# Kernel tuning notes

Hardware: AMD Instinct MI355X
Metric: run time of the kernel (lower is better)

The kernel has to match this reference:

```python
import jax, jax.numpy as jnp
import numpy as np
from jax import lax

# --- model constants (match init_kwargs) ---
B = 4096
T, N_FEAT = 100, 81
KH = 7                 # cnn_kernel_height
T_MOD = T - KH + 1     # 94
M = 100                # cnn_hidden_size
P = 128                # decoder hidden size
SKIP = 10
SH = 32                # skip_hidden_size
PT = T_MOD // SKIP     # 9


def setup_inputs() -> dict:
    key = jax.random.key(0)
    ks = jax.random.split(key, 18)
    s = 0.05
    def rn(k, shape, scale=s):
        return jax.random.normal(k, shape, dtype=jnp.float32) * scale
    return {
        "enc_data": jax.random.normal(ks[0], (B, T, N_FEAT), dtype=jnp.float32),
        # Conv2d(1 -> M, kernel=(KH, N_FEAT))
        "conv_w": rn(ks[1], (M, 1, KH, N_FEAT)),
        "conv_b": rn(ks[2], (M,)),
        # TemporalAttention: W_d: Linear(2P->M, no bias), U_d: Linear(M->M, no bias), v_d: Linear(M->1, no bias)
        "Wd": rn(ks[3], (M, 2 * P)),
        "Ud": rn(ks[4], (M, M)),
        "vd": rn(ks[5], (1, M)),
        # LSTM(input=M, hidden=P), PyTorch gate order i,f,g,o
        "lstm_wih": rn(ks[6], (4 * P, M)),
        "lstm_whh": rn(ks[7], (4 * P, P)),
        "lstm_bih": rn(ks[8], (4 * P,)),
        "lstm_bhh": rn(ks[9], (4 * P,)),
        # GRU(input=M, hidden=SH), PyTorch gate order r,z,n
        "gru_wih": rn(ks[10], (3 * SH, M)),
        "gru_whh": rn(ks[11], (3 * SH, SH)),
        "gru_bih": rn(ks[12], (3 * SH,)),
        "gru_bhh": rn(ks[13], (3 * SH,)),
        # output head: Linear(M+P+SKIP*SH -> P), ReLU, (Dropout=eval identity), Linear(P -> 1)
        "out1_w": rn(ks[14], (P, M + P + SKIP * SH)),
        "out1_b": rn(ks[15], (P,)),
        "out2_w": rn(ks[16], (1, P)),
        "out2_b": rn(ks[17], (1,)),
    }


def reference(enc_data, conv_w, conv_b, Wd, Ud, vd,
              lstm_wih, lstm_whh, lstm_bih, lstm_bhh,
              gru_wih, gru_whh, gru_bih, gru_bhh,
              out1_w, out1_b, out2_w, out2_b):
    b = enc_data.shape[0]

    # --- CNN encoder: Conv2d valid over full feature width -> [B, T_MOD, M] ---
    x = enc_data[:, None]  # [B,1,T,n]
    h = lax.conv_general_dilated(x, conv_w, window_strides=(1, 1), padding='VALID',
                                 dimension_numbers=('NCHW', 'OIHW', 'NCHW'))  # [B,M,T_MOD,1]
    H = jax.nn.relu(h + conv_b[None, :, None, None])[..., 0].transpose(0, 2, 1)  # [B,T_MOD,M]

    # precompute U_d(H) once (same math; U_d applied to H is step-invariant)
    HU = jnp.einsum('btm,km->btk', H, Ud)  # [B,T_MOD,M]

    def dec_step(carry, _):
        d, s = carry  # each [B,P]
        q = jnp.concatenate([d, s], axis=1)                       # [B,2P]
        e = jnp.tanh((q @ Wd.T)[:, None, :] + HU)                 # [B,T_MOD,M]
        scores = jnp.einsum('btm,m->bt', e, vd[0])                # [B,T_MOD]
        beta = jax.nn.softmax(scores, axis=1)                     # softmax over time
        c = jnp.einsum('bt,btm->bm', beta, H)                     # context [B,M]
        gates = c @ lstm_wih.T + lstm_bih + d @ lstm_whh.T + lstm_bhh
        i_g, f_g, g_g, o_g = jnp.split(gates, 4, axis=1)
        s_new = jax.nn.sigmoid(f_g) * s + jax.nn.sigmoid(i_g) * jnp.tanh(g_g)
        d_new = jax.nn.sigmoid(o_g) * jnp.tanh(s_new)
        return (d_new, s_new), (beta, c)

    d0 = jnp.zeros((b, P), dtype=enc_data.dtype)
    s0 = jnp.zeros((b, P), dtype=enc_data.dtype)
    (d_T, _), (betas, cs) = lax.scan(dec_step, (d0, s0), None, length=T_MOD)
    c_last = cs[-1]                                               # [B,M]
    dec_out = jnp.concatenate([d_T, c_last], axis=1)              # [B, P+M]

    # --- skip GRU over strided conv features ---
    Hs = H[:, -PT * SKIP:, :]                                     # [B, PT*SKIP, M]
    Hs = (Hs.transpose(0, 2, 1)                                   # [B, M, PT*SKIP]
            .reshape(b, M, PT, SKIP)
            .transpose(2, 0, 3, 1)                                # [PT, B, SKIP, M]
            .reshape(PT, b * SKIP, M))

    def gru_step(hprev, xt):
        gi = xt @ gru_wih.T + gru_bih
        gh = hprev @ gru_whh.T + gru_bhh
        ir, iz, inn = jnp.split(gi, 3, axis=1)
        hr, hz, hn = jnp.split(gh, 3, axis=1)
        r = jax.nn.sigmoid(ir + hr)
        z = jax.nn.sigmoid(iz + hz)
        nn_ = jnp.tanh(inn + r * hn)
        hnew = (1.0 - z) * nn_ + z * hprev
        return hnew, None

    h0 = jnp.zeros((b * SKIP, SH), dtype=enc_data.dtype)
    h_skip, _ = lax.scan(gru_step, h0, Hs)                        # [B*SKIP, SH]
    h_skip = h_skip.reshape(b, SKIP * SH)                         # matches torch view

    feat = jnp.concatenate([dec_out, h_skip], axis=1)             # [B, P+M+SKIP*SH]
    out = jax.nn.relu(feat @ out1_w.T + out1_b) @ out2_w.T + out2_b  # [B,1]
    return out[:, 0]
```

## Files before the change

### kernel.cpp

```cpp
#include <hip/hip_runtime.h>

typedef unsigned int u32;
typedef unsigned short u16;
typedef _Float16 half2_t __attribute__((ext_vector_type(2)));

#define TM 94
#define NB 2
#define DEC_NT 512

__device__ __forceinline__ float bf2f(u16 v){ return __builtin_bit_cast(float, ((u32)v)<<16); }
__device__ __forceinline__ float bflo(u32 v){ return __builtin_bit_cast(float, v<<16); }
__device__ __forceinline__ float bfhi(u32 v){ return __builtin_bit_cast(float, v & 0xffff0000u); }
__device__ __forceinline__ u32 f2bf_bits(float f){ u32 u=__builtin_bit_cast(u32,f); return (u + 0x7fffu + ((u>>16)&1u))>>16; }
__device__ __forceinline__ u32 packbf2(float a, float b){ return f2bf_bits(a) | (f2bf_bits(b)<<16); }
__device__ __forceinline__ u32 packh2(float a, float b){ half2_t h; h.x=(_Float16)a; h.y=(_Float16)b; return __builtin_bit_cast(u32,h); }
__device__ __forceinline__ float fdot2(u32 a, u32 b, float c){
  return __builtin_amdgcn_fdot2(__builtin_bit_cast(half2_t,a), __builtin_bit_cast(half2_t,b), c, false);
}
__device__ __forceinline__ float fast_rcp(float x){ return __builtin_amdgcn_rcpf(x); }
__device__ __forceinline__ float sigmoid_f(float x){ return fast_rcp(1.f + __expf(-x)); }
__device__ __forceinline__ float tanh_f(float x){ float e=__expf(2.f*x); return 1.f - 2.f*fast_rcp(e+1.f); }

__global__ __launch_bounds__(256)
void prep_kernel(const float* __restrict__ wih, const float* __restrict__ whh,
                 const float* __restrict__ Wd, const float* __restrict__ cw,
                 uint4* __restrict__ WgT, uint4* __restrict__ WdT2,
                 float* __restrict__ cwT2)
{
  int idx = blockIdx.x*256 + threadIdx.x;
  if (idx < 16384){
    int t = idx & 1023;
    int j = idx >> 10;
    int h = t >> 9, g = t & 511;
    u32 r[4];
    #pragma unroll
    for (int s=0;s<4;s++){
      int u = 4*j + s;
      u32 v = 0u;
      if (h==0){ if (u < 50) v = packh2(wih[g*100+2*u], wih[g*100+2*u+1]); }
      else     { if (u < 64) v = packh2(whh[g*128+2*u], whh[g*128+2*u+1]); }
      r[s]=v;
    }
    WgT[idx] = make_uint4(r[0],r[1],r[2],r[3]);
  } else if (idx < 20480){
    int idx2 = idx - 16384;
    int t = idx2 & 511;
    int i = idx2 >> 9;
    int mw = t >> 2, part = t & 3;
    u32 r[4] = {0u,0u,0u,0u};
    if (mw < 100){
      int ii = (i + 2*part) & 7;
      const float* wd = Wd + mw*256 + 2*(part*32 + ii*4);
      #pragma unroll
      for (int k=0;k<4;k++) r[k] = packh2(wd[2*k], wd[2*k+1]);
    }
    WdT2[idx2] = make_uint4(r[0],r[1],r[2],r[3]);
  } else if (idx < 20480 + 56700){
    int idx2 = idx - 20480;
    int c = idx2 / 5670;
    int r = idx2 - c*5670;
    int j = r / 10;
    int k = r - j*10;
    cwT2[idx2] = cw[(size_t)(10*c + k)*567 + j];
  }
}

__global__ __launch_bounds__(128)
void conv_kernel(const float* __restrict__ enc, const float* __restrict__ cwT2,
                 const float* __restrict__ cb, u16* __restrict__ Hb)
{
  __shared__ float sE[8100];
  const int tid = threadIdx.x;
  const int b = blockIdx.y;
  const int chunk = blockIdx.x;
  const float* ep = enc + (size_t)b*8100;
  for (int i=tid;i<8100;i+=128) sE[i]=ep[i];
  __syncthreads();
  if (tid >= TM) return;
  const int t = tid;
  const int mo = chunk*10;
  const float* wb = cwT2 + chunk*5670;
  float acc[10];
  #pragma unroll
  for (int k=0;k<10;k++) acc[k]=cb[mo+k];
  const float* e = sE + t*81;
  #pragma unroll 3
  for (int j=0;j<567;j++){
    float ev = e[j];
    const float* w = wb + j*10;
    #pragma unroll
    for (int k=0;k<10;k++) acc[k] += ev*w[k];
  }
  u32* out = (u32*)Hb + ((size_t)b*9400 + t*100 + mo)/2;
  #pragma unroll
  for (int k=0;k<5;k++) out[k] = packbf2(fmaxf(acc[2*k],0.f), fmaxf(acc[2*k+1],0.f));
}

#define OFF_SHU 37600
#define OFF_SQ  75200
#define OFF_SZ  76224
#define OFF_SVD 77248
#define OFF_AB  77648
#define DEC_LDS 79696

__global__ __launch_bounds__(DEC_NT) __attribute__((amdgpu_waves_per_eu(2, 4)))
void decoder_kernel(const u16* __restrict__ Hb, const float* __restrict__ Ud,
                    const float* __restrict__ vd,
                    const uint4* __restrict__ WgT, const uint4* __restrict__ WdT2,
                    const float* __restrict__ bih, const float* __restrict__ bhh,
                    float* __restrict__ dT, float* __restrict__ cLast)
{
  extern __shared__ char smem[];
  u16*      sH   = (u16*)smem;
  u16*      sHU  = (u16*)(smem + OFF_SHU);
  u32*      sq32 = (u32*)(smem + OFF_SQ);
  _Float16* sq16 = (_Float16*)(smem + OFF_SQ);
  u32*      sz32 = (u32*)(smem + OFF_SZ);
  _Float16* sz16 = (_Float16*)(smem + OFF_SZ);
  float*    svd  = (float*)(smem + OFF_SVD);
  float*    sa   = (float*)(smem + OFF_AB);
  float*    sbeta= (float*)(smem + OFF_AB + 800);
  _Float16* sg16 = (_Float16*)(smem + OFF_AB);

  const int tid = threadIdx.x;
  const int b0 = blockIdx.x * NB;

  {
    const uint4* src = (const uint4*)(Hb + (size_t)b0*9400);
    uint4* dst = (uint4*)sH;
    for (int i=tid;i<2350;i+=DEC_NT) dst[i]=src[i];
  }
  if (tid < 100) svd[tid] = vd[tid];
  for (int i=tid;i<NB*128;i+=DEC_NT){ sq32[i]=0u; sz32[i]=0u; }
  __syncthreads();

  for (int idx=tid; idx<4700; idx+=DEC_NT){
    int kq = idx/188;
    int r  = idx - kq*188;
    int bi = r/94;
    int t  = r - 94*bi;
    const u32* hrow = (const u32*)sH + bi*4700 + t*50;
    const float* ud0 = Ud + (kq*4+0)*100;
    const float* ud1 = Ud + (kq*4+1)*100;
    const float* ud2 = Ud + (kq*4+2)*100;
    const float* ud3 = Ud + (kq*4+3)*100;
    float c0=0.f,c1=0.f,c2=0.f,c3=0.f;
    #pragma unroll 5
    for (int mq=0; mq<25; mq++){
      uint2 hp = *(const uint2*)(hrow + mq*2);
      float h0=bflo(hp.x), h1=bfhi(hp.x), h2=bflo(hp.y), h3=bfhi(hp.y);
      float4 u0 = *(const float4*)(ud0 + mq*4);
      float4 u1 = *(const float4*)(ud1 + mq*4);
      float4 u2 = *(const float4*)(ud2 + mq*4);
      float4 u3 = *(const float4*)(ud3 + mq*4);
      c0 += h0*u0.x + h1*u0.y + h2*u0.z + h3*u0.w;
      c1 += h0*u1.x + h1*u1.y + h2*u1.z + h3*u1.w;
      c2 += h0*u2.x + h1*u2.y + h2*u2.z + h3*u2.w;
      c3 += h0*u3.x + h1*u3.y + h2*u3.z + h3*u3.w;
    }
    u32* dst = (u32*)sHU + bi*4700 + t*50 + kq*2;
    dst[0] = packbf2(c0,c1);
    dst[1] = packbf2(c2,c3);
  }
  __syncthreads();

  const int mw = tid>>2, part = tid&3;
  uint4 wv[8];
  if (mw < 100){
    #pragma unroll
    for (int i=0;i<8;i++) wv[i] = WdT2[i*512 + tid];
  }
  const float biasg = bih[tid] + bhh[tid];
  const uint4* wp0 = WgT + tid;
  const uint4* wp1 = WgT + 512 + tid;

  float s_reg = 0.f;

  #pragma unroll 1
  for (int step=0; step<TM; step++){
    if (mw < 100){
      #pragma unroll 1
      for (int bi=0;bi<NB;bi++){
        const u32* qb = sq32 + bi*128 + part*32;
        float a0=0.f, a1=0.f;
        #pragma unroll
        for (int i=0;i<8;i++){
          int ii = (i+2*part)&7;
          uint4 qv = *(const uint4*)(qb + ii*4);
          a0 = fdot2(wv[i].x, qv.x, a0);
          a1 = fdot2(wv[i].y, qv.y, a1);
          a0 = fdot2(wv[i].z, qv.z, a0);
          a1 = fdot2(wv[i].w, qv.w, a1);
        }
        float acc = a0+a1;
        acc += __shfl_xor(acc,1);
        acc += __shfl_xor(acc,2);
        if (part==0) sa[bi*100+mw]=acc;
      }
    }
    __syncthreads();
    if (tid < NB*188){
      int row = tid>>1, th = tid&1;
      int bi = row/94;
      int t  = row - 94*bi;
      const uint4* hu4 = (const uint4*)((const u32*)sHU + bi*4700 + t*50 + th*24);
      const float4* ap = (const float4*)(sa + bi*100) + th*12;
      const float4* vp = (const float4*)svd + th*12;
      float acc=0.f;
      #pragma unroll
      for (int c=0;c<6;c++){
        uint4 h4 = hu4[c];
        float4 a0 = ap[2*c], a1 = ap[2*c+1];
        float4 v0 = vp[2*c], v1 = vp[2*c+1];
        acc += v0.x*tanh_f(a0.x + bflo(h4.x));
        acc += v0.y*tanh_f(a0.y + bfhi(h4.x));
        acc += v0.z*tanh_f(a0.z + bflo(h4.y));
        acc += v0.w*tanh_f(a0.w + bfhi(h4.y));
        acc += v1.x*tanh_f(a1.x + bflo(h4.z));
        acc += v1.y*tanh_f(a1.y + bfhi(h4.z));
        acc += v1.z*tanh_f(a1.z + bflo(h4.w));
        acc += v1.w*tanh_f(a1.w + bfhi(h4.w));
      }
      if (th){
        uint2 ht = *(const uint2*)((const u32*)hu4 + 24);
        float4 a = ap[12]; float4 v = vp[12];
        acc += v.x*tanh_f(a.x + bflo(ht.x));
        acc += v.y*tanh_f(a.y + bfhi(ht.x));
        acc += v.z*tanh_f(a.z + bflo(ht.y));
        acc += v.w*tanh_f(a.w + bfhi(ht.y));
      }
      acc += __shfl_xor(acc,1);
      if (!th) sbeta[bi*96+t]=acc;
    }
    __syncthreads();
    if (tid < 64*NB){
      int bi = tid>>6, lane = tid&63;
      float s0 = sbeta[bi*96+lane];
      float s1 = (lane<30)? sbeta[bi*96+64+lane] : -1e30f;
      float mx = fmaxf(s0,s1);
      #pragma unroll
      for (int o=32;o>=1;o>>=1) mx = fmaxf(mx, __shfl_xor(mx,o));
      float e0 = __expf(s0-mx);
      float e1 = (lane<30)? __expf(s1-mx) : 0.f;
      float sm = e0+e1;
      #pragma unroll
      for (int o=32;o>=1;o>>=1) sm += __shfl_xor(sm,o);
      float rs = fast_rcp(sm);
      sbeta[bi*96+lane] = e0*rs;
      if (lane<30) sbeta[bi*96+64+lane] = e1*rs;
    }
    __syncthreads();
    if (tid < NB*200){
      int bi = tid/200;
      int r  = tid - 200*bi;
      int mp = r>>2, th = r&3;
      int tstart = (th<2) ? th*24 : 48+(th-2)*23;
      const float* bp = sbeta + bi*96 + tstart;
      const u32* hp = (const u32*)sH + bi*4700 + tstart*50 + mp;
      float a0=0.f, a1=0.f;
      #pragma unroll
      for (int i=0;i<23;i++){
        float be = bp[i];
        u32 h = hp[i*50];
        a0 += be*bflo(h); a1 += be*bfhi(h);
      }
      if (th<2){
        float be = bp[23]; u32 h = hp[23*50];
        a0 += be*bflo(h); a1 += be*bfhi(h);
      }
      a0 += __shfl_xor(a0,1); a1 += __shfl_xor(a1,1);
      a0 += __shfl_xor(a0,2); a1 += __shfl_xor(a1,2);
      if (th==0){
        sz32[bi*128+mp] = packh2(a0,a1);
        if (step==TM-1){
          cLast[(size_t)(b0+bi)*100 + 2*mp]   = a0;
          cLast[(size_t)(b0+bi)*100 + 2*mp+1] = a1;
        }
      }
    }
    __syncthreads();
    {
      float acc0 = biasg, acc1 = biasg;
      const u32* zc0 = sz32;
      const u32* zc1 = sz32 + 128;
      #pragma unroll 1
      for (int jb=0; jb<16; jb+=4){
        uint4 w[4], v[4];
        #pragma unroll
        for (int k=0;k<4;k++) w[k] = wp0[(jb+k)*1024];
        #pragma unroll
        for (int k=0;k<4;k++) v[k] = wp1[(jb+k)*1024];
        #pragma unroll
        for (int k=0;k<4;k++){
          int j = jb+k;
          uint4 zA0 = *(const uint4*)(zc0 + 4*j);
          uint4 zA1 = *(const uint4*)(zc1 + 4*j);
          acc0 = fdot2(w[k].x, zA0.x, acc0); acc0 = fdot2(w[k].y, zA0.y, acc0);
          acc0 = fdot2(w[k].z, zA0.z, acc0); acc0 = fdot2(w[k].w, zA0.w, acc0);
          acc1 = fdot2(w[k].x, zA1.x, acc1); acc1 = fdot2(w[k].y, zA1.y, acc1);
          acc1 = fdot2(w[k].z, zA1.z, acc1); acc1 = fdot2(w[k].w, zA1.w, acc1);
          uint4 zB0 = *(const uint4*)(zc0 + 64 + 4*j);
          uint4 zB1 = *(const uint4*)(zc1 + 64 + 4*j);
          acc0 = fdot2(v[k].x, zB0.x, acc0); acc0 = fdot2(v[k].y, zB0.y, acc0);
          acc0 = fdot2(v[k].z, zB0.z, acc0); acc0 = fdot2(v[k].w, zB0.w, acc0);
          acc1 = fdot2(v[k].x, zB1.x, acc1); acc1 = fdot2(v[k].y, zB1.y, acc1);
          acc1 = fdot2(v[k].z, zB1.z, acc1); acc1 = fdot2(v[k].w, zB1.w, acc1);
        }
      }
      sg16[      tid] = (_Float16)acc0;
      sg16[512 + tid] = (_Float16)acc1;
    }
    __syncthreads();
    if (tid < 128*NB){
      int bi = tid>>7, p = tid&127;
      float ig = (float)sg16[bi*512+p];
      float fg = (float)sg16[bi*512+128+p];
      float gg_= (float)sg16[bi*512+256+p];
      float og = (float)sg16[bi*512+384+p];
      float sn = sigmoid_f(fg)*s_reg + sigmoid_f(ig)*tanh_f(gg_);
      float dn = sigmoid_f(og)*tanh_f(sn);
      s_reg = sn;
      sq16[bi*256+p]      = (_Float16)dn;
      sq16[bi*256+128+p]  = (_Float16)sn;
      sz16[bi*256+128+p]  = (_Float16)dn;
      if (step==TM-1) dT[(size_t)(b0+bi)*128+p]=dn;
    }
    __syncthreads();
  }
}

__global__ __launch_bounds__(256)
void gru_kernel(const u16* __restrict__ Hb, const float* __restrict__ wih,
                const float* __restrict__ whh, const float* __restrict__ bihp,
                const float* __restrict__ bhhp, float* __restrict__ hskip)
{
  __shared__ float sWih[96][101];
  __shared__ float sWhh[96][33];
  __shared__ float sxt[8][100];
  __shared__ float sh[8][33];
  const int tid = threadIdx.x;
  for (int i=tid;i<9600;i+=256){ sWih[i/100][i%100]=wih[i]; }
  for (int i=tid;i<3072;i+=256){ sWhh[i>>5][i&31]=whh[i]; }
  const int r = tid>>5, j = tid&31;
  const int rowg = blockIdx.x*8 + r;
  const int b = rowg/10, sk = rowg - b*10;
  const float b_r = bihp[j], b_z = bihp[32+j], b_n = bihp[64+j];
  const float hb_r = bhhp[j], hb_z = bhhp[32+j], hb_n = bhhp[64+j];
  sh[r][j]=0.f;
  float h = 0.f;
  __syncthreads();
  for (int pt=0; pt<9; pt++){
    for (int i=tid;i<800;i+=256){
      int rr=i/100, m=i-rr*100;
      int rg = blockIdx.x*8+rr; int bb=rg/10, ss=rg-bb*10;
      sxt[rr][m] = bf2f(Hb[(size_t)bb*9400 + (size_t)(4+pt*10+ss)*100 + m]);
    }
    __syncthreads();
    float gi_r=b_r, gi_z=b_z, gi_n=b_n, gh_r=hb_r, gh_z=hb_z, gh_n=hb_n;
    #pragma unroll 4
    for (int m=0;m<100;m++){
      float x = sxt[r][m];
      gi_r += sWih[j][m]*x; gi_z += sWih[32+j][m]*x; gi_n += sWih[64+j][m]*x;
    }
    #pragma unroll
    for (int k=0;k<32;k++){
      float hp = sh[r][k];
      gh_r += sWhh[j][k]*hp; gh_z += sWhh[32+j][k]*hp; gh_n += sWhh[64+j][k]*hp;
    }
    float rg_ = sigmoid_f(gi_r+gh_r);
    float z  = sigmoid_f(gi_z+gh_z);
    float n  = tanh_f(gi_n + rg_*gh_n);
    h = (1.f-z)*n + z*h;
    __syncthreads();
    sh[r][j]=h;
    __syncthreads();
  }
  hskip[(size_t)b*320 + sk*32 + j] = h;
}

#define OUT_NB 32
#define OUT_LDS ((OUT_NB*552 + 8*552)*4)

__global__ __launch_bounds__(256)
void out_kernel(const float* __restrict__ dT, const float* __restrict__ cLast,
                const float* __restrict__ hskip, const float* __restrict__ w1,
                const float* __restrict__ b1, const float* __restrict__ w2,
                const float* __restrict__ b2, float* __restrict__ outp)
{
  extern __shared__ float osm[];
  float* sf = osm;
  float* sw = osm + OUT_NB*552;
  const int tid = threadIdx.x;
  const int b0 = blockIdx.x*OUT_NB;
  for (int i=tid;i<OUT_NB*548;i+=256){
    int bl = i/548, k = i - 548*bl; int b = b0+bl;
    float v;
    if (k<128) v = dT[(size_t)b*128+k];
    else if (k<228) v = cLast[(size_t)b*100+(k-128)];
    else v = hskip[(size_t)b*320+(k-228)];
    sf[bl*552+k]=v;
  }
  const int bl = tid>>3, j = tid&7;
  float outv = 0.f;
  for (int jt=0; jt<128; jt+=8){
    __syncthreads();
    for (int i=tid;i<8*548;i+=256){
      int rr=i/548, c=i-548*rr;
      sw[rr*552+c] = w1[(size_t)jt*548 + i];
    }
    __syncthreads();
    float acc = b1[jt+j];
    const float* fr = sf + bl*552;
    const float* wr = sw + j*552;
    #pragma unroll 4
    for (int k=0;k<548;k++) acc += fr[k]*wr[k];
    outv += fmaxf(acc,0.f)*w2[jt+j];
  }
  outv += __shfl_xor(outv,1);
  outv += __shfl_xor(outv,2);
  outv += __shfl_xor(outv,4);
  if (j==0) outp[b0+bl] = outv + b2[0];
}

extern "C" void kernel_launch(void* const* d_in, const int* in_sizes, int n_in,
                              void* d_out, int out_size, void* d_ws, size_t ws_size,
                              hipStream_t stream)
{
  const float* enc      = (const float*)d_in[0];
  const float* conv_w   = (const float*)d_in[1];
  const float* conv_b   = (const float*)d_in[2];
  const float* Wd       = (const float*)d_in[3];
  const float* Ud       = (const float*)d_in[4];
  const float* vd       = (const float*)d_in[5];
  const float* lstm_wih = (const float*)d_in[6];
  const float* lstm_whh = (const float*)d_in[7];
  const float* lstm_bih = (const float*)d_in[8];
  const float* lstm_bhh = (const float*)d_in[9];
  const float* gru_wih  = (const float*)d_in[10];
  const float* gru_whh  = (const float*)d_in[11];
  const float* gru_bih  = (const float*)d_in[12];
  const float* gru_bhh  = (const float*)d_in[13];
  const float* out1_w   = (const float*)d_in[14];
  const float* out1_b   = (const float*)d_in[15];
  const float* out2_w   = (const float*)d_in[16];
  const float* out2_b   = (const float*)d_in[17];

  char* ws = (char*)d_ws;
  u16*   Hb    = (u16*)ws;
  float* dT    = (float*)(ws + 77004800);
  float* cLast = (float*)(ws + 79101952);
  float* hskip = (float*)(ws + 80740352);
  uint4* WgT   = (uint4*)(ws + 80740352);
  uint4* WdT2  = (uint4*)(ws + 81002496);
  float* cwT2  = (float*)(ws + 81068032);

  prep_kernel<<<302, 256, 0, stream>>>(lstm_wih, lstm_whh, Wd, conv_w,
                                       WgT, WdT2, cwT2);

  conv_kernel<<<dim3(10,4096,1), 128, 0, stream>>>(enc, cwT2, conv_b, Hb);

  (void)hipFuncSetAttribute((const void*)decoder_kernel,
                            hipFuncAttributeMaxDynamicSharedMemorySize, DEC_LDS);
  decoder_kernel<<<4096/NB, DEC_NT, DEC_LDS, stream>>>(Hb, Ud, vd, WgT, WdT2,
                                                       lstm_bih, lstm_bhh,
                                                       dT, cLast);

  gru_kernel<<<5120, 256, 0, stream>>>(Hb, gru_wih, gru_whh, gru_bih, gru_bhh, hskip);

  (void)hipFuncSetAttribute((const void*)out_kernel,
                            hipFuncAttributeMaxDynamicSharedMemorySize, OUT_LDS);
  out_kernel<<<4096/OUT_NB, 256, OUT_LDS, stream>>>(dT, cLast, hskip, out1_w, out1_b,
                                                    out2_w, out2_b, (float*)d_out);
}
```

Baseline: 7.346 ms.

## Fold softmax into context pass and fuse LSTM gate epilogue via shuffles

The separate softmax phase becomes an unnormalised exp of the attention score, with the sum accumulated alongside the context reduction and divided out at the end, which removes one barrier and the max/sum reductions. Threads are remapped so each quad holds the i,f,g,o gates for one hidden unit. The quad exchanges them with shuffles instead of a shared-memory round-trip, which removes another barrier. The decoder-state copy in the z buffer is double-buffered by step parity to avoid a write-after-read hazard. Skipping the max subtraction risks overflow in exp if scores grow large, and the new gate-to-thread mapping changes the weight access pattern.

```diff
diff --git a/kernel.cpp b/kernel.cpp
--- a/kernel.cpp
+++ b/kernel.cpp
@@ -99,9 +99,9 @@
 #define OFF_SHU 37600
 #define OFF_SQ  75200
 #define OFF_SZ  76224
-#define OFF_SVD 77248
-#define OFF_AB  77648
-#define DEC_LDS 79696
+#define OFF_SVD 77760
+#define OFF_AB  78160
+#define DEC_LDS 79728
 
 __global__ __launch_bounds__(DEC_NT) __attribute__((amdgpu_waves_per_eu(2, 4)))
 void decoder_kernel(const u16* __restrict__ Hb, const float* __restrict__ Ud,
@@ -116,11 +116,9 @@
   u32*      sq32 = (u32*)(smem + OFF_SQ);
   _Float16* sq16 = (_Float16*)(smem + OFF_SQ);
   u32*      sz32 = (u32*)(smem + OFF_SZ);
-  _Float16* sz16 = (_Float16*)(smem + OFF_SZ);
   float*    svd  = (float*)(smem + OFF_SVD);
   float*    sa   = (float*)(smem + OFF_AB);
   float*    sbeta= (float*)(smem + OFF_AB + 800);
-  _Float16* sg16 = (_Float16*)(smem + OFF_AB);
 
   const int tid = threadIdx.x;
   const int b0 = blockIdx.x * NB;
@@ -131,7 +129,8 @@
     for (int i=tid;i<2350;i+=DEC_NT) dst[i]=src[i];
   }
   if (tid < 100) svd[tid] = vd[tid];
-  for (int i=tid;i<NB*128;i+=DEC_NT){ sq32[i]=0u; sz32[i]=0u; }
+  for (int i=tid;i<NB*128;i+=DEC_NT) sq32[i]=0u;
+  for (int i=tid;i<NB*192;i+=DEC_NT) sz32[i]=0u;
   __syncthreads();
 
   for (int idx=tid; idx<4700; idx+=DEC_NT){
@@ -170,9 +169,11 @@
     #pragma unroll
     for (int i=0;i<8;i++) wv[i] = WdT2[i*512 + tid];
   }
-  const float biasg = bih[tid] + bhh[tid];
-  const uint4* wp0 = WgT + tid;
-  const uint4* wp1 = WgT + 512 + tid;
+  const int p5 = tid>>2, gid = tid&3;
+  const int g5 = gid*128 + p5;
+  const float biasg = bih[g5] + bhh[g5];
+  const uint4* wp0 = WgT + g5;
+  const uint4* wp1 = WgT + 512 + g5;
 
   float s_reg = 0.f;
 
@@ -230,24 +231,7 @@
         acc += v.w*tanh_f(a.w + bfhi(ht.y));
       }
       acc += __shfl_xor(acc,1);
-      if (!th) sbeta[bi*96+t]=acc;
-    }
-    __syncthreads();
-    if (tid < 64*NB){
-      int bi = tid>>6, lane = tid&63;
-      float s0 = sbeta[bi*96+lane];
-      float s1 = (lane<30)? sbeta[bi*96+64+lane] : -1e30f;
-      float mx = fmaxf(s0,s1);
-      #pragma unroll
-      for (int o=32;o>=1;o>>=1) mx = fmaxf(mx, __shfl_xor(mx,o));
-      float e0 = __expf(s0-mx);
-      float e1 = (lane<30)? __expf(s1-mx) : 0.f;
-      float sm = e0+e1;
-      #pragma unroll
-      for (int o=32;o>=1;o>>=1) sm += __shfl_xor(sm,o);
-      float rs = fast_rcp(sm);
-      sbeta[bi*96+lane] = e0*rs;
-      if (lane<30) sbeta[bi*96+64+lane] = e1*rs;
+      if (!th) sbeta[bi*96+t]=__expf(acc);
     }
     __syncthreads();
     if (tid < NB*200){
@@ -257,21 +241,23 @@
       int tstart = (th<2) ? th*24 : 48+(th-2)*23;
       const float* bp = sbeta + bi*96 + tstart;
       const u32* hp = (const u32*)sH + bi*4700 + tstart*50 + mp;
-      float a0=0.f, a1=0.f;
+      float a0=0.f, a1=0.f, asum=0.f;
       #pragma unroll
       for (int i=0;i<23;i++){
         float be = bp[i];
         u32 h = hp[i*50];
-        a0 += be*bflo(h); a1 += be*bfhi(h);
+        a0 += be*bflo(h); a1 += be*bfhi(h); asum += be;
       }
       if (th<2){
         float be = bp[23]; u32 h = hp[23*50];
-        a0 += be*bflo(h); a1 += be*bfhi(h);
-      }
-      a0 += __shfl_xor(a0,1); a1 += __shfl_xor(a1,1);
-      a0 += __shfl_xor(a0,2); a1 += __shfl_xor(a1,2);
+        a0 += be*bflo(h); a1 += be*bfhi(h); asum += be;
+      }
+      a0 += __shfl_xor(a0,1); a1 += __shfl_xor(a1,1); asum += __shfl_xor(asum,1);
+      a0 += __shfl_xor(a0,2); a1 += __shfl_xor(a1,2); asum += __shfl_xor(asum,2);
       if (th==0){
-        sz32[bi*128+mp] = packh2(a0,a1);
+        float rs = fast_rcp(asum);
+        a0 *= rs; a1 *= rs;
+        sz32[bi*192+mp] = packh2(a0,a1);
         if (step==TM-1){
           cLast[(size_t)(b0+bi)*100 + 2*mp]   = a0;
           cLast[(size_t)(b0+bi)*100 + 2*mp+1] = a1;
@@ -282,7 +268,8 @@
     {
       float acc0 = biasg, acc1 = biasg;
       const u32* zc0 = sz32;
-      const u32* zc1 = sz32 + 128;
+      const u32* zc1 = sz32 + 192;
+      const int dof = 64 + (step&1)*64;
       #pragma unroll 1
       for (int jb=0; jb<16; jb+=4){
         uint4 w[4], v[4];
@@ -299,31 +286,34 @@
           acc0 = fdot2(w[k].z, zA0.z, acc0); acc0 = fdot2(w[k].w, zA0.w, acc0);
           acc1 = fdot2(w[k].x, zA1.x, acc1); acc1 = fdot2(w[k].y, zA1.y, acc1);
           acc1 = fdot2(w[k].z, zA1.z, acc1); acc1 = fdot2(w[k].w, zA1.w, acc1);
-          uint4 zB0 = *(const uint4*)(zc0 + 64 + 4*j);
-          uint4 zB1 = *(const uint4*)(zc1 + 64 + 4*j);
+          uint4 zB0 = *(const uint4*)(zc0 + dof + 4*j);
+          uint4 zB1 = *(const uint4*)(zc1 + dof + 4*j);
           acc0 = fdot2(v[k].x, zB0.x, acc0); acc0 = fdot2(v[k].y, zB0.y, acc0);
           acc0 = fdot2(v[k].z, zB0.z, acc0); acc0 = fdot2(v[k].w, zB0.w, acc0);
           acc1 = fdot2(v[k].x, zB1.x, acc1); acc1 = fdot2(v[k].y, zB1.y, acc1);
           acc1 = fdot2(v[k].z, zB1.z, acc1); acc1 = fdot2(v[k].w, zB1.w, acc1);
         }
       }
-      sg16[      tid] = (_Float16)acc0;
-      sg16[512 + tid] = (_Float16)acc1;
-    }
-    __syncthreads();
-    if (tid < 128*NB){
-      int bi = tid>>7, p = tid&127;
-      float ig = (float)sg16[bi*512+p];
-      float fg = (float)sg16[bi*512+128+p];
-      float gg_= (float)sg16[bi*512+256+p];
-      float og = (float)sg16[bi*512+384+p];
+      float x0 = __shfl_xor(acc0,1), x1 = __shfl_xor(acc1,1);
+      float lo0 = (gid&1)? x0:acc0, hi0 = (gid&1)? acc0:x0;
+      float lo1 = (gid&1)? x1:acc1, hi1 = (gid&1)? acc1:x1;
+      float lo0b = __shfl_xor(lo0,2), hi0b = __shfl_xor(hi0,2);
+      float lo1b = __shfl_xor(lo1,2), hi1b = __shfl_xor(hi1,2);
+      const bool hib = (gid>=2);
+      float ig  = hib ? lo1b : lo0;
+      float fg  = hib ? hi1b : hi0;
+      float gg_ = hib ? lo1  : lo0b;
+      float og  = hib ? hi1  : hi0b;
       float sn = sigmoid_f(fg)*s_reg + sigmoid_f(ig)*tanh_f(gg_);
       float dn = sigmoid_f(og)*tanh_f(sn);
       s_reg = sn;
-      sq16[bi*256+p]      = (_Float16)dn;
-      sq16[bi*256+128+p]  = (_Float16)sn;
-      sz16[bi*256+128+p]  = (_Float16)dn;
-      if (step==TM-1) dT[(size_t)(b0+bi)*128+p]=dn;
+      if ((gid&1)==0){
+        int bi = gid>>1;
+        sq16[bi*256+p5]     = (_Float16)dn;
+        sq16[bi*256+128+p5] = (_Float16)sn;
+        ((_Float16*)(sz32 + bi*192 + 64 + ((step&1)^1)*64))[p5] = (_Float16)dn;
+        if (step==TM-1) dT[(size_t)(b0+bi)*128+p5]=dn;
+      }
     }
     __syncthreads();
   }
```

Result: slower. 9.785 ms (+33.2%).
